# Performance work log

Measured on AMD Instinct MI355X. Metric: run time of the kernel, lower is better.

## Reference

```python
import jax, jax.numpy as jnp
import numpy as np

NX = 41                      # cube side: 2*r_max/voxel + 1 with r_max=6.0, voxel=0.3
VOXEL = 0.3
R_MAX = 6.0
MIN_DIST = 0.8
MIN_SEP = max(1, int(round(MIN_DIST / VOXEL)))   # 3 voxels
K = 4                        # topk_per_channel
NEG = -1.0e9                 # fp32 sentinel used by the torch module
VALID_THRESH = -1.0e8


def setup_inputs() -> dict:
    key = jax.random.key(0)
    B, N, C = 1, 128, 4
    G = NX ** 3
    ax = np.arange(NX)
    ii, jj, kk = np.meshgrid(ax, ax, ax, indexing='ij')
    coords = np.stack([ii, jj, kk], axis=-1).reshape(-1, 3)          # [G,3] integer voxel coords
    center = (NX - 1) / 2.0
    grid_xyz = ((coords - center) * VOXEL).astype(np.float32)        # [G,3] local Angstrom coords
    sphere_mask = np.linalg.norm(grid_xyz, axis=-1) <= R_MAX         # [G] bool
    k1, k2, k3 = jax.random.split(key, 3)
    density = jax.random.normal(k1, (B, N, C, G), jnp.float32)
    A = jax.random.normal(k2, (B, N, 3, 3), jnp.float32)
    Rmats, _ = jnp.linalg.qr(A)                                      # proper-ish rotation matrices
    tpos = jax.random.normal(k3, (B, N, 3), jnp.float32)
    node_mask = jnp.ones((B, N), jnp.float32)
    return dict(density=density,
                grid_xyz=jnp.asarray(grid_xyz),
                sphere_mask=jnp.asarray(sphere_mask),
                coords_int=jnp.asarray(coords, jnp.int32),
                Rmats=Rmats, tpos=tpos, node_mask=node_mask)


def extract_peaks(density, grid_xyz, sphere_mask, coords_int):
    # density: [B,N,C,G]; iterative argmax peak-picking with Chebyshev NMS suppression.
    v0 = jnp.where(sphere_mask[None, None, None, :], density, NEG)
    cx = coords_int[:, 0][None, None, None, :]   # [1,1,1,G]
    cy = coords_int[:, 1][None, None, None, :]
    cz = coords_int[:, 2][None, None, None, :]

    def step(v, _):
        idx = jnp.argmax(v, axis=-1)                                   # [B,N,C]
        score = jnp.take_along_axis(v, idx[..., None], axis=-1)[..., 0]
        valid = score > VALID_THRESH
        xyz = grid_xyz[idx]                                            # [B,N,C,3]
        ijk = coords_int[idx]                                          # [B,N,C,3]
        # Chebyshev (max-abs) voxel distance to the picked peak, per axis to avoid a [.,G,3] temp
        d = jnp.maximum(jnp.maximum(jnp.abs(cx - ijk[..., 0:1]),
                                    jnp.abs(cy - ijk[..., 1:2])),
                        jnp.abs(cz - ijk[..., 2:3]))                    # [B,N,C,G]
        suppress = (d <= MIN_SEP) & valid[..., None]
        v = jnp.where(suppress, NEG, v)
        out = (jnp.where(valid, score, NEG),
               jnp.where(valid[..., None], xyz, 0.0),
               valid)
        return v, out

    _, (scores, xyz, mask) = jax.lax.scan(step, v0, None, length=K)
    # K is leading scan axis -> move to axis 3 giving [B,N,C,K,...]
    return (jnp.moveaxis(xyz, 0, 3), jnp.moveaxis(scores, 0, 3), jnp.moveaxis(mask, 0, 3))


def reference(density, grid_xyz, sphere_mask, coords_int, Rmats, tpos, node_mask):
    peaks_xyz, peaks_score, peaks_mask = extract_peaks(density, grid_xyz, sphere_mask, coords_int)
    # local -> global frame: R @ x + t
    coords_global = jnp.einsum('bnij,bnckj->bncki', Rmats, peaks_xyz) + tpos[:, :, None, None, :]
    m = node_mask[..., None, None, None]                                # [B,N,1,1,1]
    coords_local = peaks_xyz * m
    coords_global = coords_global * m
    scores = peaks_score * node_mask[..., None, None]
    mask = peaks_mask & node_mask.astype(bool)[..., None, None]
    return coords_local, coords_global, scores, mask
```

## Files before the change

kernel.cpp:

```cpp
#include <hip/hip_runtime.h>

#define G_VOX  68921
#define NSEG   272
#define MWORDS 2176
#define NEGV (-1.0e9f)
#define VTH  (-1.0e8f)

__device__ __forceinline__ bool sphere_bit(const float* __restrict__ grid_xyz, int e) {
    if (e >= G_VOX) return false;
    float gx = grid_xyz[e * 3 + 0];
    float gy = grid_xyz[e * 3 + 1];
    float gz = grid_xyz[e * 3 + 2];
    float s  = __fadd_rn(__fadd_rn(__fmul_rn(gx, gx), __fmul_rn(gy, gy)),
                         __fmul_rn(gz, gz));
    return (__fsqrt_rn(s) <= 6.0f);
}

__global__ __launch_bounds__(256) void build_mask(
    const float* __restrict__ grid_xyz,
    unsigned int* __restrict__ mask,
    unsigned short* __restrict__ rm)
{
    const int tid = threadIdx.x;
    const int lane = tid & 63;

    {
        int idx = blockIdx.x * 256 + tid;
        unsigned long long bal = __ballot(sphere_bit(grid_xyz, idx));
        if (lane == 0)       mask[idx >> 5] = (unsigned int)bal;
        else if (lane == 32) mask[idx >> 5] = (unsigned int)(bal >> 32);
    }
    {
        int v = blockIdx.x * 256 + tid;
        int e = (v & ~255) + ((v >> 4) & 15) + 16 * (v & 15);
        unsigned long long bal = __ballot(sphere_bit(grid_xyz, e));
        if ((lane & 15) == 0)
            rm[v >> 4] = (unsigned short)((bal >> ((lane >> 4) << 4)) & 0xFFFFull);
    }
}

__global__ __launch_bounds__(256) void seg_max(
    const float* __restrict__ density, const unsigned short* __restrict__ rm,
    float* __restrict__ svals, int* __restrict__ sidxs)
{
    const int nc  = blockIdx.x;
    const int c   = blockIdx.y;
    const int tid = threadIdx.x;
    const int p   = tid & 15;
    const int sl  = tid >> 4;
    const int base = c * 4096 + sl * 256 + p;
    const float* dens = density + (size_t)nc * G_VOX;

    const unsigned int bits = rm[c * 256 + tid];

    float bv = NEGV;
    int   bi = base;
    if (c < 16) {
        #pragma unroll
        for (int j = 0; j < 16; ++j) {
            int e = base + 16 * j;
            float d = dens[e];
            float v = ((bits >> j) & 1u) ? d : NEGV;
            if (v > bv) { bv = v; bi = e; }
        }
    } else {
        #pragma unroll
        for (int j = 0; j < 16; ++j) {
            int e = base + 16 * j;
            if (e < G_VOX) {
                float d = dens[e];
                float v = ((bits >> j) & 1u) ? d : NEGV;
                if (v > bv) { bv = v; bi = e; }
            }
        }
    }
    #pragma unroll
    for (int off = 1; off < 16; off <<= 1) {
        float ov = __shfl_xor(bv, off);
        int   oi = __shfl_xor(bi, off);
        if (ov > bv || (ov == bv && oi < bi)) { bv = ov; bi = oi; }
    }
    if (p == 0) {
        int s = c * 16 + sl;
        svals[nc * NSEG + s] = bv;
        sidxs[nc * NSEG + s] = bi;
    }
}

__global__ __launch_bounds__(256) void pick_peaks(
    const float* __restrict__ density,
    const float* __restrict__ grid_xyz,
    const unsigned int* __restrict__ mask,
    const float* __restrict__ svals, const int* __restrict__ sidxs,
    const float* __restrict__ Rm, const float* __restrict__ tp,
    const float* __restrict__ nmask,
    float* __restrict__ out)
{
    __shared__ float sval[NSEG];
    __shared__ int   sidx[NSEG];
    __shared__ unsigned int smask[MWORDS];
    __shared__ int   flag[NSEG];
    __shared__ int   list[128];
    __shared__ int   nlist;
    __shared__ float rv[4];
    __shared__ int   ri[4];
    __shared__ float pval[4];
    __shared__ int   pidx[4];
    __shared__ int   pcoord[3];

    const int tid = threadIdx.x;
    const int nc  = blockIdx.x;
    const int n   = nc >> 2;
    const float* dens = density + (size_t)nc * G_VOX;

    for (int i = tid; i < NSEG; i += 256) {
        sval[i] = svals[nc * NSEG + i];
        sidx[i] = sidxs[nc * NSEG + i];
        flag[i] = 0;
    }
    for (int i = tid; i < MWORDS; i += 256) smask[i] = mask[i];
    __syncthreads();

    for (int p = 0; p < 4; ++p) {
        float bv = -INFINITY;
        int   bi = 0x7FFFFFFF;
        for (int s = tid; s < NSEG; s += 256) {
            float v = sval[s];
            int   i = sidx[s];
            if (v > bv || (v == bv && i < bi)) { bv = v; bi = i; }
        }
        for (int off = 32; off > 0; off >>= 1) {
            float ov = __shfl_down(bv, off);
            int   oi = __shfl_down(bi, off);
            if (ov > bv || (ov == bv && oi < bi)) { bv = ov; bi = oi; }
        }
        if ((tid & 63) == 0) { rv[tid >> 6] = bv; ri[tid >> 6] = bi; }
        __syncthreads();
        if (tid == 0) {
            for (int wv = 1; wv < 4; ++wv) {
                if (rv[wv] > bv || (rv[wv] == bv && ri[wv] < bi)) { bv = rv[wv]; bi = ri[wv]; }
            }
            pval[p] = bv;
            pidx[p] = bi;
            int pi = bi / 1681;
            int rr = bi - pi * 1681;
            int pj = rr / 41;
            pcoord[0] = pi; pcoord[1] = pj; pcoord[2] = rr - pj * 41;
            nlist = 0;
        }
        __syncthreads();

        if (p < 3 && pval[p] > VTH) {
            if (tid < 49) {
                int di = tid / 7 - 3, dj = tid % 7 - 3;
                int ii = pcoord[0] + di, jj = pcoord[1] + dj;
                if (ii >= 0 && ii <= 40 && jj >= 0 && jj <= 40) {
                    int k0 = pcoord[2] - 3; if (k0 < 0)  k0 = 0;
                    int k1 = pcoord[2] + 3; if (k1 > 40) k1 = 40;
                    int b0  = ii * 1681 + jj * 41 + k0;
                    int cnt = k1 - k0 + 1;
                    unsigned long long m = ((1ull << cnt) - 1ull) << (b0 & 31);
                    int w0 = b0 >> 5;
                    atomicAnd(&smask[w0], ~(unsigned int)m);
                    unsigned int hi = (unsigned int)(m >> 32);
                    if (hi) atomicAnd(&smask[w0 + 1], ~hi);
                    int s0 = b0 >> 8;
                    int s1 = (b0 + cnt - 1) >> 8;
                    if (atomicMax(&flag[s0], p + 1) < p + 1) {
                        int q = atomicAdd(&nlist, 1); list[q] = s0;
                    }
                    if (s1 != s0 && atomicMax(&flag[s1], p + 1) < p + 1) {
                        int q = atomicAdd(&nlist, 1); list[q] = s1;
                    }
                }
            }
            __syncthreads();
            const int lane = tid & 63;
            const int wv   = tid >> 6;
            const int cnt  = nlist;
            for (int j = wv; j < cnt; j += 4) {
                int s = list[j];
                float v = NEGV;
                int bi2 = s * 256 + lane * 4;
                #pragma unroll
                for (int q = 0; q < 4; ++q) {
                    int e = s * 256 + lane * 4 + q;
                    if (e < G_VOX) {
                        float d = dens[e];
                        unsigned int w = smask[e >> 5];
                        float vv = ((w >> (e & 31)) & 1u) ? d : NEGV;
                        if (vv > v) { v = vv; bi2 = e; }
                    }
                }
                for (int off = 32; off > 0; off >>= 1) {
                    float ov = __shfl_down(v, off);
                    int   oi = __shfl_down(bi2, off);
                    if (ov > v || (ov == v && oi < bi2)) { v = ov; bi2 = oi; }
                }
                if (lane == 0) { sval[s] = v; sidx[s] = bi2; }
            }
        }
        __syncthreads();
    }

    if (tid < 4) {
        const int k   = tid;
        const float val = pval[k];
        const int   idx = pidx[k];
        const bool valid = val > VTH;
        float gx = 0.0f, gy = 0.0f, gz = 0.0f;
        if (valid) {
            gx = grid_xyz[idx * 3 + 0];
            gy = grid_xyz[idx * 3 + 1];
            gz = grid_xyz[idx * 3 + 2];
        }
        const float nm = nmask[n];
        const float* R = Rm + n * 9;
        const float* t = tp + n * 3;
        float wx = R[0] * gx + R[1] * gy + R[2] * gz + t[0];
        float wy = R[3] * gx + R[4] * gy + R[5] * gz + t[1];
        float wz = R[6] * gx + R[7] * gy + R[8] * gz + t[2];

        const size_t o3 = ((size_t)nc * 4 + k) * 3;
        out[o3 + 0] = gx * nm;
        out[o3 + 1] = gy * nm;
        out[o3 + 2] = gz * nm;
        out[6144 + o3 + 0] = wx * nm;
        out[6144 + o3 + 1] = wy * nm;
        out[6144 + o3 + 2] = wz * nm;
        const size_t o1 = (size_t)nc * 4 + k;
        out[12288 + o1] = (valid ? val : NEGV) * nm;
        out[14336 + o1] = (valid && nm != 0.0f) ? 1.0f : 0.0f;
    }
}

extern "C" void kernel_launch(void* const* d_in, const int* in_sizes, int n_in,
                              void* d_out, int out_size, void* d_ws, size_t ws_size,
                              hipStream_t stream) {
    const float* density  = (const float*)d_in[0];
    const float* grid_xyz = (const float*)d_in[1];
    const float* Rm    = (const float*)d_in[4];
    const float* tpos  = (const float*)d_in[5];
    const float* nmask = (const float*)d_in[6];
    float* out = (float*)d_out;

    unsigned int*   mask = (unsigned int*)d_ws;
    unsigned short* rm   = (unsigned short*)((char*)d_ws + 8704);
    float* svals = (float*)((char*)d_ws + 17408);
    int*   sidxs = (int*)  ((char*)d_ws + 17408 + (size_t)512 * NSEG * 4);

    build_mask<<<dim3(272), dim3(256), 0, stream>>>(grid_xyz, mask, rm);
    seg_max<<<dim3(512, 17), dim3(256), 0, stream>>>(density, rm, svals, sidxs);
    pick_peaks<<<dim3(512), dim3(256), 0, stream>>>(density, grid_xyz, mask,
                                                    svals, sidxs, Rm, tpos, nmask, out);
}
```

Baseline: 245.0 us.

## Vectorize density loads with alignment-shifted segments and recompute suppression arithmetically

Each (n,c) density row starts at an offset of nc*68921 floats, which is misaligned by a varying amount. Segments are therefore shifted by h = (-nc)&3 so seg_max and the rescan can use aligned float4 loads. The sphere bit table is rebuilt in four phase variants to match. pick_peaks no longer copies the 8.7KB mask into shared memory or updates it with atomics; it instead tests each voxel's Chebyshev distance to the earlier peaks on the fly, reading the global mask. This trades shared-memory traffic and atomics for per-element integer divides and extra global mask reads.

```diff
diff --git a/kernel.cpp b/kernel.cpp
--- a/kernel.cpp
+++ b/kernel.cpp
@@ -1,46 +1,56 @@
 #include <hip/hip_runtime.h>
 
 #define G_VOX  68921
+#define GMAX   68920
 #define NSEG   272
+#define NRSEG  270
 #define MWORDS 2176
+#define RMQ_N  4320
 #define NEGV (-1.0e9f)
 #define VTH  (-1.0e8f)
 
-__device__ __forceinline__ bool sphere_bit(const float* __restrict__ grid_xyz, int e) {
-    if (e >= G_VOX) return false;
-    float gx = grid_xyz[e * 3 + 0];
-    float gy = grid_xyz[e * 3 + 1];
-    float gz = grid_xyz[e * 3 + 2];
+__device__ __forceinline__ bool sphere_bit(const float* __restrict__ gxyz, int e) {
+    if (e >= G_VOX || e < 0) return false;
+    float gx = gxyz[e * 3 + 0];
+    float gy = gxyz[e * 3 + 1];
+    float gz = gxyz[e * 3 + 2];
     float s  = __fadd_rn(__fadd_rn(__fmul_rn(gx, gx), __fmul_rn(gy, gy)),
                          __fmul_rn(gz, gz));
     return (__fsqrt_rn(s) <= 6.0f);
 }
 
 __global__ __launch_bounds__(256) void build_mask(
-    const float* __restrict__ grid_xyz,
+    const float* __restrict__ gxyz,
     unsigned int* __restrict__ mask,
-    unsigned short* __restrict__ rm)
+    unsigned short* __restrict__ rmq)
 {
-    const int tid = threadIdx.x;
+    const int tid  = threadIdx.x;
     const int lane = tid & 63;
-
     {
         int idx = blockIdx.x * 256 + tid;
-        unsigned long long bal = __ballot(sphere_bit(grid_xyz, idx));
+        unsigned long long bal = __ballot(sphere_bit(gxyz, idx));
         if (lane == 0)       mask[idx >> 5] = (unsigned int)bal;
         else if (lane == 32) mask[idx >> 5] = (unsigned int)(bal >> 32);
     }
-    {
-        int v = blockIdx.x * 256 + tid;
-        int e = (v & ~255) + ((v >> 4) & 15) + 16 * (v & 15);
-        unsigned long long bal = __ballot(sphere_bit(grid_xyz, e));
-        if ((lane & 15) == 0)
-            rm[v >> 4] = (unsigned short)((bal >> ((lane >> 4) << 4)) & 0xFFFFull);
+    int gid = blockIdx.x * 256 + tid;
+    if (gid < 4 * RMQ_N) {
+        int h   = gid / RMQ_N;
+        int rem = gid - h * RMQ_N;
+        int s   = rem >> 4;
+        int p   = rem & 15;
+        int base = h + s * 256 + 4 * p;
+        unsigned int bits = 0;
+        #pragma unroll
+        for (int j = 0; j < 4; ++j)
+            #pragma unroll
+            for (int u = 0; u < 4; ++u)
+                if (sphere_bit(gxyz, base + 64 * j + u)) bits |= 1u << (j * 4 + u);
+        rmq[gid] = (unsigned short)bits;
     }
 }
 
 __global__ __launch_bounds__(256) void seg_max(
-    const float* __restrict__ density, const unsigned short* __restrict__ rm,
+    const float* __restrict__ density, const unsigned short* __restrict__ rmq,
     float* __restrict__ svals, int* __restrict__ sidxs)
 {
     const int nc  = blockIdx.x;
@@ -48,29 +58,51 @@
     const int tid = threadIdx.x;
     const int p   = tid & 15;
     const int sl  = tid >> 4;
-    const int base = c * 4096 + sl * 256 + p;
+    const int s   = c * 16 + sl;
+    const int h   = (-nc) & 3;
     const float* dens = density + (size_t)nc * G_VOX;
 
-    const unsigned int bits = rm[c * 256 + tid];
+    const unsigned int bits = (s < NRSEG) ? (unsigned int)rmq[h * RMQ_N + s * 16 + p] : 0u;
+    const int base = h + s * 256 + 4 * p;
 
     float bv = NEGV;
     int   bi = base;
     if (c < 16) {
         #pragma unroll
-        for (int j = 0; j < 16; ++j) {
-            int e = base + 16 * j;
-            float d = dens[e];
-            float v = ((bits >> j) & 1u) ? d : NEGV;
-            if (v > bv) { bv = v; bi = e; }
+        for (int j = 0; j < 4; ++j) {
+            int e = base + 64 * j;
+            float4 d = *reinterpret_cast<const float4*>(dens + e);
+            float v0 = ((bits >> (j * 4 + 0)) & 1u) ? d.x : NEGV;
+            float v1 = ((bits >> (j * 4 + 1)) & 1u) ? d.y : NEGV;
+            float v2 = ((bits >> (j * 4 + 2)) & 1u) ? d.z : NEGV;
+            float v3 = ((bits >> (j * 4 + 3)) & 1u) ? d.w : NEGV;
+            if (v0 > bv) { bv = v0; bi = e;     }
+            if (v1 > bv) { bv = v1; bi = e + 1; }
+            if (v2 > bv) { bv = v2; bi = e + 2; }
+            if (v3 > bv) { bv = v3; bi = e + 3; }
         }
     } else {
         #pragma unroll
-        for (int j = 0; j < 16; ++j) {
-            int e = base + 16 * j;
-            if (e < G_VOX) {
-                float d = dens[e];
-                float v = ((bits >> j) & 1u) ? d : NEGV;
-                if (v > bv) { bv = v; bi = e; }
+        for (int j = 0; j < 4; ++j) {
+            int e = base + 64 * j;
+            if (e + 3 <= GMAX) {
+                float4 d = *reinterpret_cast<const float4*>(dens + e);
+                float v0 = ((bits >> (j * 4 + 0)) & 1u) ? d.x : NEGV;
+                float v1 = ((bits >> (j * 4 + 1)) & 1u) ? d.y : NEGV;
+                float v2 = ((bits >> (j * 4 + 2)) & 1u) ? d.z : NEGV;
+                float v3 = ((bits >> (j * 4 + 3)) & 1u) ? d.w : NEGV;
+                if (v0 > bv) { bv = v0; bi = e;     }
+                if (v1 > bv) { bv = v1; bi = e + 1; }
+                if (v2 > bv) { bv = v2; bi = e + 2; }
+                if (v3 > bv) { bv = v3; bi = e + 3; }
+            } else {
+                #pragma unroll
+                for (int u = 0; u < 4; ++u) {
+                    if ((bits >> (j * 4 + u)) & 1u) {
+                        float v = dens[e + u];
+                        if (v > bv) { bv = v; bi = e + u; }
+                    }
+                }
             }
         }
     }
@@ -81,7 +113,6 @@
         if (ov > bv || (ov == bv && oi < bi)) { bv = ov; bi = oi; }
     }
     if (p == 0) {
-        int s = c * 16 + sl;
         svals[nc * NSEG + s] = bv;
         sidxs[nc * NSEG + s] = bi;
     }
@@ -89,8 +120,8 @@
 
 __global__ __launch_bounds__(256) void pick_peaks(
     const float* __restrict__ density,
-    const float* __restrict__ grid_xyz,
-    const unsigned int* __restrict__ mask,
+    const float* __restrict__ gxyz,
+    const unsigned int* __restrict__ maskg,
     const float* __restrict__ svals, const int* __restrict__ sidxs,
     const float* __restrict__ Rm, const float* __restrict__ tp,
     const float* __restrict__ nmask,
@@ -98,19 +129,19 @@
 {
     __shared__ float sval[NSEG];
     __shared__ int   sidx[NSEG];
-    __shared__ unsigned int smask[MWORDS];
     __shared__ int   flag[NSEG];
-    __shared__ int   list[128];
+    __shared__ int   list[104];
     __shared__ int   nlist;
     __shared__ float rv[4];
     __shared__ int   ri[4];
     __shared__ float pval[4];
     __shared__ int   pidx[4];
-    __shared__ int   pcoord[3];
+    __shared__ int   pki[4], pkj[4], pkk[4];
 
     const int tid = threadIdx.x;
     const int nc  = blockIdx.x;
     const int n   = nc >> 2;
+    const int h   = (-nc) & 3;
     const float* dens = density + (size_t)nc * G_VOX;
 
     for (int i = tid; i < NSEG; i += 256) {
@@ -118,7 +149,6 @@
         sidx[i] = sidxs[nc * NSEG + i];
         flag[i] = 0;
     }
-    for (int i = tid; i < MWORDS; i += 256) smask[i] = mask[i];
     __syncthreads();
 
     for (int p = 0; p < 4; ++p) {
@@ -137,15 +167,14 @@
         if ((tid & 63) == 0) { rv[tid >> 6] = bv; ri[tid >> 6] = bi; }
         __syncthreads();
         if (tid == 0) {
-            for (int wv = 1; wv < 4; ++wv) {
-                if (rv[wv] > bv || (rv[wv] == bv && ri[wv] < bi)) { bv = rv[wv]; bi = ri[wv]; }
-            }
+            for (int w = 1; w < 4; ++w)
+                if (rv[w] > bv || (rv[w] == bv && ri[w] < bi)) { bv = rv[w]; bi = ri[w]; }
             pval[p] = bv;
             pidx[p] = bi;
             int pi = bi / 1681;
             int rr = bi - pi * 1681;
             int pj = rr / 41;
-            pcoord[0] = pi; pcoord[1] = pj; pcoord[2] = rr - pj * 41;
+            pki[p] = pi; pkj[p] = pj; pkk[p] = rr - pj * 41;
             nlist = 0;
         }
         __syncthreads();
@@ -153,19 +182,14 @@
         if (p < 3 && pval[p] > VTH) {
             if (tid < 49) {
                 int di = tid / 7 - 3, dj = tid % 7 - 3;
-                int ii = pcoord[0] + di, jj = pcoord[1] + dj;
+                int ii = pki[p] + di, jj = pkj[p] + dj;
                 if (ii >= 0 && ii <= 40 && jj >= 0 && jj <= 40) {
-                    int k0 = pcoord[2] - 3; if (k0 < 0)  k0 = 0;
-                    int k1 = pcoord[2] + 3; if (k1 > 40) k1 = 40;
-                    int b0  = ii * 1681 + jj * 41 + k0;
-                    int cnt = k1 - k0 + 1;
-                    unsigned long long m = ((1ull << cnt) - 1ull) << (b0 & 31);
-                    int w0 = b0 >> 5;
-                    atomicAnd(&smask[w0], ~(unsigned int)m);
-                    unsigned int hi = (unsigned int)(m >> 32);
-                    if (hi) atomicAnd(&smask[w0 + 1], ~hi);
-                    int s0 = b0 >> 8;
-                    int s1 = (b0 + cnt - 1) >> 8;
+                    int k0 = pkk[p] - 3; if (k0 < 0)  k0 = 0;
+                    int k1 = pkk[p] + 3; if (k1 > 40) k1 = 40;
+                    int b0 = ii * 1681 + jj * 41 + k0;
+                    int b1 = b0 + (k1 - k0);
+                    int s0 = (b0 > h) ? (b0 - h) >> 8 : 0;
+                    int s1 = (b1 > h) ? (b1 - h) >> 8 : 0;
                     if (atomicMax(&flag[s0], p + 1) < p + 1) {
                         int q = atomicAdd(&nlist, 1); list[q] = s0;
                     }
@@ -176,28 +200,50 @@
             }
             __syncthreads();
             const int lane = tid & 63;
-            const int wv   = tid >> 6;
+            const int w    = tid >> 6;
             const int cnt  = nlist;
-            for (int j = wv; j < cnt; j += 4) {
-                int s = list[j];
-                float v = NEGV;
-                int bi2 = s * 256 + lane * 4;
+            for (int j = w; j < cnt; j += 4) {
+                int s  = list[j];
+                int e0 = h + s * 256 + 4 * lane;
+                bool vec = (e0 + 3 <= GMAX);
+                float4 d = make_float4(0.f, 0.f, 0.f, 0.f);
+                if (vec) d = *reinterpret_cast<const float4*>(dens + e0);
+                float bv2 = NEGV;
+                int   bi2 = e0;
                 #pragma unroll
-                for (int q = 0; q < 4; ++q) {
-                    int e = s * 256 + lane * 4 + q;
-                    if (e < G_VOX) {
-                        float d = dens[e];
-                        unsigned int w = smask[e >> 5];
-                        float vv = ((w >> (e & 31)) & 1u) ? d : NEGV;
-                        if (vv > v) { v = vv; bi2 = e; }
+                for (int u = 0; u < 4; ++u) {
+                    int e = e0 + u;
+                    if (e <= GMAX) {
+                        unsigned int wrd = maskg[e >> 5];
+                        if ((wrd >> (e & 31)) & 1u) {
+                            int ei = e / 1681;
+                            int er = e - ei * 1681;
+                            int ej = er / 41;
+                            int ek = er - ej * 41;
+                            bool sup = false;
+                            for (int q = 0; q <= p; ++q) {
+                                if (pval[q] > VTH) {
+                                    int ai = abs(ei - pki[q]);
+                                    int aj = abs(ej - pkj[q]);
+                                    int ak = abs(ek - pkk[q]);
+                                    int m = ai > aj ? ai : aj; m = m > ak ? m : ak;
+                                    if (m <= 3) sup = true;
+                                }
+                            }
+                            if (!sup) {
+                                float v = vec ? (u == 0 ? d.x : u == 1 ? d.y : u == 2 ? d.z : d.w)
+                                              : dens[e];
+                                if (v > bv2) { bv2 = v; bi2 = e; }
+                            }
+                        }
                     }
                 }
                 for (int off = 32; off > 0; off >>= 1) {
-                    float ov = __shfl_down(v, off);
+                    float ov = __shfl_down(bv2, off);
                     int   oi = __shfl_down(bi2, off);
-                    if (ov > v || (ov == v && oi < bi2)) { v = ov; bi2 = oi; }
+                    if (ov > bv2 || (ov == bv2 && oi < bi2)) { bv2 = ov; bi2 = oi; }
                 }
-                if (lane == 0) { sval[s] = v; sidx[s] = bi2; }
+                if (lane == 0) { sval[s] = bv2; sidx[s] = bi2; }
             }
         }
         __syncthreads();
@@ -210,9 +256,9 @@
         const bool valid = val > VTH;
         float gx = 0.0f, gy = 0.0f, gz = 0.0f;
         if (valid) {
-            gx = grid_xyz[idx * 3 + 0];
-            gy = grid_xyz[idx * 3 + 1];
-            gz = grid_xyz[idx * 3 + 2];
+            gx = gxyz[idx * 3 + 0];
+            gy = gxyz[idx * 3 + 1];
+            gz = gxyz[idx * 3 + 2];
         }
         const float nm = nmask[n];
         const float* R = Rm + n * 9;
@@ -245,12 +291,12 @@
     float* out = (float*)d_out;
 
     unsigned int*   mask = (unsigned int*)d_ws;
-    unsigned short* rm   = (unsigned short*)((char*)d_ws + 8704);
-    float* svals = (float*)((char*)d_ws + 17408);
-    int*   sidxs = (int*)  ((char*)d_ws + 17408 + (size_t)512 * NSEG * 4);
-
-    build_mask<<<dim3(272), dim3(256), 0, stream>>>(grid_xyz, mask, rm);
-    seg_max<<<dim3(512, 17), dim3(256), 0, stream>>>(density, rm, svals, sidxs);
+    unsigned short* rmq  = (unsigned short*)((char*)d_ws + 8704);
+    float* svals = (float*)((char*)d_ws + 43264);
+    int*   sidxs = (int*)  ((char*)d_ws + 600320);
+
+    build_mask<<<dim3(272), dim3(256), 0, stream>>>(grid_xyz, mask, rmq);
+    seg_max<<<dim3(512, 17), dim3(256), 0, stream>>>(density, rmq, svals, sidxs);
     pick_peaks<<<dim3(512), dim3(256), 0, stream>>>(density, grid_xyz, mask,
                                                     svals, sidxs, Rm, tpos, nmask, out);
 }
```

After: 261.9 us. +6.9%, slower.
